# Kernel optimization log

Hardware: AMD Instinct MI355X
Metric: run time of the kernel (lower is better)

Reference implementation:

```python
import jax, jax.numpy as jnp
import numpy as np

INPUT_SIZE = 64
HIDDEN = 128
BATCH = 512
SEQ = 512


def setup_inputs() -> dict:
    key = jax.random.key(0)
    ks = jax.random.split(key, 7)
    s_ih = 1.0 / np.sqrt(HIDDEN)
    token = jax.random.normal(ks[0], (BATCH, SEQ, INPUT_SIZE), dtype=jnp.float32)
    W_ih = jax.random.uniform(ks[1], (HIDDEN, INPUT_SIZE), jnp.float32, -s_ih, s_ih)
    W_hh = jax.random.uniform(ks[2], (HIDDEN, HIDDEN), jnp.float32, -s_ih, s_ih)
    b_ih = jax.random.uniform(ks[3], (HIDDEN,), jnp.float32, -s_ih, s_ih)
    b_hh = jax.random.uniform(ks[4], (HIDDEN,), jnp.float32, -s_ih, s_ih)
    W_lin = jax.random.uniform(ks[5], (1, HIDDEN), jnp.float32, -s_ih, s_ih)
    b_lin = jax.random.uniform(ks[6], (1,), jnp.float32, -s_ih, s_ih)
    return {"token": token, "W_ih": W_ih, "W_hh": W_hh, "b_ih": b_ih,
            "b_hh": b_hh, "W_lin": W_lin, "b_lin": b_lin}


def reference(token, W_ih, W_hh, b_ih, b_hh, W_lin, b_lin):
    # Precompute input projection for all timesteps: [T, B, H]
    x_proj = jnp.einsum('bti,hi->tbh', token, W_ih) + b_ih + b_hh
    h0 = jnp.zeros((token.shape[0], W_hh.shape[0]), dtype=token.dtype)

    def step(h, xp):
        h_new = jnp.tanh(xp + h @ W_hh.T)
        return h_new, None

    h_last, _ = jax.lax.scan(step, h0, x_proj)
    # Linear head on last hidden state: [B, 1]
    return h_last @ W_lin.T + b_lin
```

## Files before the change

kernel.cpp:

```cpp
#include <hip/hip_runtime.h>

#define B_ 512
#define T_ 512
#define I_ 64
#define H_ 128
#define CHUNK 64
#define NCHUNK (T_ / CHUNK)

#define TOKBYTES 16384
#define HB0      (2 * TOKBYTES)
#define HB1      (HB0 + 512)
#define DUMMY    (HB1 + 512)
#define LDS_SZ   (DUMMY + 256)

__device__ __forceinline__ void gload_lds16(const float* g, void* l) {
    __builtin_amdgcn_global_load_lds(
        (const __attribute__((address_space(1))) unsigned int*)g,
        (__attribute__((address_space(3))) unsigned int*)l, 16, 0, 0);
}

#define FM(a, x, w) "v_fmac_f32 v" #a ", v" #x ", v" #w "\n\t"
#define SC(n) "v_mul_f32 v" #n ", 0x4038aa3b, v" #n "\n\t"

#define CLOBS \
    "v48","v49","v50","v51","v52","v53","v54","v55","v56","v57","v58","v59", \
    "v60","v61","v62","v63","v64","v65","v66","v67","v68","v69","v70","v71", \
    "v72","v73","v74","v75","v76","v77","v78","v79","v80","v81","v82","v83", \
    "v84","v85","v86","v87","v88","v89","v90","v91","v92","v93","v94","v95", \
    "v96","v97","v98","v99","v100","v101","v102","v103","v104","v105","v106", \
    "v107","v108","v109","v110","v111","v112","v113","v114","v115","v116", \
    "v117","v118","v119","v120","v121","v122","v123","v124","v125","v126", \
    "v127","memory"

#define RNN_STEP(TOKA, HRD, HWR, BA, BB, BC, BD, M1, M2)                      \
    asm volatile(                                                             \
        "ds_read_b128 v[56:59], %0\n\t"                                       \
        "ds_read_b128 v[64:67], %1\n\t"                                       \
        "ds_read_b128 v[68:71], %1 offset:256\n\t"                            \
        "v_add_u32 %0, 256, %0\n\t"                                           \
        "s_waitcnt lgkmcnt(2)\n\t"                                            \
        "v_fma_f32 v48, v56, v112, %3\n\t"                                    \
        "v_fma_f32 v49, v56, v116, %4\n\t"                                    \
        "v_fma_f32 v50, v56, v120, %5\n\t"                                    \
        "v_fma_f32 v51, v56, v124, %6\n\t"                                    \
        FM(48,57,113) FM(49,57,117) FM(50,57,121) FM(51,57,125)               \
        FM(48,58,114) FM(49,58,118) FM(50,58,122) FM(51,58,126)               \
        FM(48,59,115) FM(49,59,119) FM(50,59,123) FM(51,59,127)               \
        "s_waitcnt lgkmcnt(1)\n\t"                                            \
        FM(48,64,80) FM(49,64,88) FM(50,64,96)  FM(51,64,104)                 \
        FM(48,65,81) FM(49,65,89) FM(50,65,97)  FM(51,65,105)                 \
        FM(48,66,82) FM(49,66,90) FM(50,66,98)  FM(51,66,106)                 \
        FM(48,67,83) FM(49,67,91) FM(50,67,99)  FM(51,67,107)                 \
        "s_waitcnt lgkmcnt(0)\n\t"                                            \
        FM(48,68,84) FM(49,68,92) FM(50,68,100) FM(51,68,108)                 \
        FM(48,69,85) FM(49,69,93) FM(50,69,101) FM(51,69,109)                 \
        FM(48,70,86) FM(49,70,94) FM(50,70,102) FM(51,70,110)                 \
        FM(48,71,87) FM(49,71,95) FM(50,71,103) FM(51,71,111)                 \
        "s_nop 1\n\t"                                                         \
        "v_add_f32 v48, v48, v48 quad_perm:[1,0,3,2] row_mask:0xf bank_mask:0xf\n\t" \
        "v_add_f32 v49, v49, v49 quad_perm:[1,0,3,2] row_mask:0xf bank_mask:0xf\n\t" \
        "v_add_f32 v50, v50, v50 quad_perm:[1,0,3,2] row_mask:0xf bank_mask:0xf\n\t" \
        "v_add_f32 v51, v51, v51 quad_perm:[1,0,3,2] row_mask:0xf bank_mask:0xf\n\t" \
        "v_cndmask_b32 v52, v48, v49, %7\n\t"                                 \
        "v_cndmask_b32 v53, v50, v51, %7\n\t"                                 \
        "s_nop 0\n\t"                                                         \
        "v_add_f32 v52, v52, v52 quad_perm:[2,3,0,1] row_mask:0xf bank_mask:0xf\n\t" \
        "v_add_f32 v53, v53, v53 quad_perm:[2,3,0,1] row_mask:0xf bank_mask:0xf\n\t" \
        "v_cndmask_b32 v54, v52, v53, %8\n\t"                                 \
        "s_nop 1\n\t"                                                         \
        "v_add_f32 v54, v54, v54 row_shl:8 row_mask:0xf bank_mask:0x3\n\t"    \
        "s_nop 1\n\t"                                                         \
        "v_add_f32 v54, v54, v54 row_shl:4 row_mask:0xf bank_mask:0x1\n\t"    \
        "s_nop 1\n\t"                                                         \
        "v_exp_f32 v54, v54\n\t"                                              \
        "s_nop 0\n\t"                                                         \
        "v_add_f32 v54, 1.0, v54\n\t"                                         \
        "v_rcp_f32 v55, v54\n\t"                                              \
        "s_nop 0\n\t"                                                         \
        "v_fma_f32 v54, v55, -2.0, 1.0\n\t"                                   \
        "ds_write_b32 %2, v54\n\t"                                            \
        "s_waitcnt lgkmcnt(0)\n\t"                                            \
        "s_barrier"                                                           \
        : "+v"(TOKA)                                                          \
        : "v"(HRD), "v"(HWR), "v"(BA), "v"(BB), "v"(BC), "v"(BD),             \
          "s"(M1), "s"(M2)                                                    \
        : CLOBS)

__global__ __launch_bounds__(512) __attribute__((amdgpu_waves_per_eu(4, 4)))
void rnn_kernel(const float* __restrict__ token,
                const float* __restrict__ W_ih,
                const float* __restrict__ W_hh,
                const float* __restrict__ b_ih,
                const float* __restrict__ b_hh,
                const float* __restrict__ W_lin,
                const float* __restrict__ b_lin,
                float* __restrict__ out)
{
    __shared__ __align__(16) char lds[LDS_SZ];
    const unsigned lb =
        (unsigned)(uintptr_t)(__attribute__((address_space(3))) char*)lds;

    const int tid = threadIdx.x;
    const int e   = tid & 15;
    const int G   = tid >> 4;
    const int b   = blockIdx.x;
    const int jb  = 4 * G;

    {
        const float* pWh = W_hh + jb * H_ + e * 8;
        const float* pWi = W_ih + jb * I_ + e * 4;
        asm volatile(
            "global_load_dwordx4 v[80:83],   %0, off\n\t"
            "global_load_dwordx4 v[84:87],   %0, off offset:16\n\t"
            "global_load_dwordx4 v[88:91],   %0, off offset:512\n\t"
            "global_load_dwordx4 v[92:95],   %0, off offset:528\n\t"
            "global_load_dwordx4 v[96:99],   %0, off offset:1024\n\t"
            "global_load_dwordx4 v[100:103], %0, off offset:1040\n\t"
            "global_load_dwordx4 v[104:107], %0, off offset:1536\n\t"
            "global_load_dwordx4 v[108:111], %0, off offset:1552\n\t"
            "global_load_dwordx4 v[112:115], %1, off\n\t"
            "global_load_dwordx4 v[116:119], %1, off offset:256\n\t"
            "global_load_dwordx4 v[120:123], %1, off offset:512\n\t"
            "global_load_dwordx4 v[124:127], %1, off offset:768\n\t"
            "s_waitcnt vmcnt(0)\n\t"
            SC(80) SC(81) SC(82) SC(83) SC(84) SC(85) SC(86) SC(87)
            SC(88) SC(89) SC(90) SC(91) SC(92) SC(93) SC(94) SC(95)
            SC(96) SC(97) SC(98) SC(99) SC(100) SC(101) SC(102) SC(103)
            SC(104) SC(105) SC(106) SC(107) SC(108) SC(109) SC(110) SC(111)
            SC(112) SC(113) SC(114) SC(115) SC(116) SC(117) SC(118) SC(119)
            SC(120) SC(121) SC(122) SC(123) SC(124) SC(125) SC(126) SC(127)
            :: "v"(pWh), "v"(pWi) : CLOBS);
    }

    const float k16 = 2.885390081777927f / 16.0f;
    const float biasA = (b_ih[jb + 0] + b_hh[jb + 0]) * k16;
    const float biasB = (b_ih[jb + 1] + b_hh[jb + 1]) * k16;
    const float biasC = (b_ih[jb + 2] + b_hh[jb + 2]) * k16;
    const float biasD = (b_ih[jb + 3] + b_hh[jb + 3]) * k16;
    const unsigned long long M1 = 0xAAAAAAAAAAAAAAAAULL;
    const unsigned long long M2 = 0xCCCCCCCCCCCCCCCCULL;

    const int  jsel   = jb + (e & 3);
    const int  wbyte  = ((((jsel >> 2) & 1) * 16 + (jsel >> 3)) * 16) + (jsel & 3) * 4;
    const bool writer = (e < 4);
    const unsigned dmy = lb + DUMMY + (tid & 63) * 4;
    const unsigned hw0 = writer ? (lb + HB1 + wbyte) : dmy;
    const unsigned hw1 = writer ? (lb + HB0 + wbyte) : dmy;
    const unsigned hr0 = lb + HB0 + e * 16;
    const unsigned hr1 = lb + HB1 + e * 16;

    const float* tok_row = token + (size_t)b * T_ * I_;
    const int S0 = tid, S1 = 512 + tid;

    gload_lds16(tok_row + S0 * 4, lds + S0 * 16);
    gload_lds16(tok_row + S1 * 4, lds + S1 * 16);
    if (tid < H_) *(float*)(lds + HB0 + tid * 4) = 0.0f;
    asm volatile("s_waitcnt vmcnt(0) lgkmcnt(0)\n\ts_barrier" ::: "memory");

#pragma unroll 1
    for (int c = 0; c < NCHUNK; ++c) {
        const int cb = c & 1;
        const bool has_next = (c + 1 < NCHUNK);
        if (has_next) {
            const float* g = tok_row + (size_t)(c + 1) * CHUNK * I_;
            char* dst = lds + (cb ^ 1) * TOKBYTES;
            gload_lds16(g + S0 * 4, dst + S0 * 16);
            gload_lds16(g + S1 * 4, dst + S1 * 16);
        }
        unsigned toka = lb + cb * TOKBYTES + e * 16;

#pragma unroll 1
        for (int tt = 0; tt < CHUNK; tt += 2) {
            RNN_STEP(toka, hr0, hw0, biasA, biasB, biasC, biasD, M1, M2);
            RNN_STEP(toka, hr1, hw1, biasA, biasB, biasC, biasD, M1, M2);
        }

        if (has_next) {
            asm volatile("s_waitcnt vmcnt(0)\n\ts_barrier" ::: "memory");
        }
    }

    if (tid < 64) {
        const int a0 = tid, a1 = tid + 64;
        const int l0 = (((a0 >> 2) & 1) * 16 + (a0 >> 3)) * 4 + (a0 & 3);
        const int l1 = (((a1 >> 2) & 1) * 16 + (a1 >> 3)) * 4 + (a1 & 3);
        float p = *(const float*)(lds + HB0 + l0 * 4) * W_lin[a0]
                + *(const float*)(lds + HB0 + l1 * 4) * W_lin[a1];
#pragma unroll
        for (int off = 32; off; off >>= 1) p += __shfl_down(p, off);
        if (tid == 0) out[b] = p + b_lin[0];
    }
}

extern "C" void kernel_launch(void* const* d_in, const int* in_sizes, int n_in,
                              void* d_out, int out_size, void* d_ws, size_t ws_size,
                              hipStream_t stream) {
    const float* token = (const float*)d_in[0];
    const float* W_ih  = (const float*)d_in[1];
    const float* W_hh  = (const float*)d_in[2];
    const float* b_ih  = (const float*)d_in[3];
    const float* b_hh  = (const float*)d_in[4];
    const float* W_lin = (const float*)d_in[5];
    const float* b_lin = (const float*)d_in[6];
    float* out = (float*)d_out;

    hipLaunchKernelGGL(rnn_kernel, dim3(B_), dim3(512), 0, stream,
                       token, W_ih, W_hh, b_ih, b_hh, W_lin, b_lin, out);
}
```

Before: 206.8 us.

## Stream token inputs directly into registers with a 4-deep global-load ring

Drops the chunked double-buffered global-to-LDS token staging. Each lane now keeps a four-timestep ring of token vectors in VGPRs and issues global_load_dwordx4 directly, waiting on vmcnt(3) so loads run three steps ahead. This removes the per-step LDS token read, the per-chunk barriers and 32KB of LDS. In exchange it exposes per-step global latency, which is only hidden if three steps of prefetch are enough. The offset wraps with a mask, so the last three loads fetch harmless wrapped addresses.

Result: faster. 197.9 us, median of 2 (-4.3%).

```diff
diff --git a/kernel.cpp b/kernel.cpp
--- a/kernel.cpp
+++ b/kernel.cpp
@@ -4,20 +4,11 @@
 #define T_ 512
 #define I_ 64
 #define H_ 128
-#define CHUNK 64
-#define NCHUNK (T_ / CHUNK)
 
-#define TOKBYTES 16384
-#define HB0      (2 * TOKBYTES)
-#define HB1      (HB0 + 512)
-#define DUMMY    (HB1 + 512)
-#define LDS_SZ   (DUMMY + 256)
-
-__device__ __forceinline__ void gload_lds16(const float* g, void* l) {
-    __builtin_amdgcn_global_load_lds(
-        (const __attribute__((address_space(1))) unsigned int*)g,
-        (__attribute__((address_space(3))) unsigned int*)l, 16, 0, 0);
-}
+#define HB0    0
+#define HB1    512
+#define DUMMY  1024
+#define LDS_SZ 1280
 
 #define FM(a, x, w) "v_fmac_f32 v" #a ", v" #x ", v" #w "\n\t"
 #define SC(n) "v_mul_f32 v" #n ", 0x4038aa3b, v" #n "\n\t"
@@ -32,30 +23,31 @@
     "v117","v118","v119","v120","v121","v122","v123","v124","v125","v126", \
     "v127","memory"
 
-#define RNN_STEP(TOKA, HRD, HWR, BA, BB, BC, BD, M1, M2)                      \
+#define RNN_STEP(TA, TB, TC, TD, HRD, HWR)                                    \
     asm volatile(                                                             \
-        "ds_read_b128 v[56:59], %0\n\t"                                       \
-        "ds_read_b128 v[64:67], %1\n\t"                                       \
-        "ds_read_b128 v[68:71], %1 offset:256\n\t"                            \
-        "v_add_u32 %0, 256, %0\n\t"                                           \
-        "s_waitcnt lgkmcnt(2)\n\t"                                            \
-        "v_fma_f32 v48, v56, v112, %3\n\t"                                    \
-        "v_fma_f32 v49, v56, v116, %4\n\t"                                    \
-        "v_fma_f32 v50, v56, v120, %5\n\t"                                    \
-        "v_fma_f32 v51, v56, v124, %6\n\t"                                    \
-        FM(48,57,113) FM(49,57,117) FM(50,57,121) FM(51,57,125)               \
-        FM(48,58,114) FM(49,58,118) FM(50,58,122) FM(51,58,126)               \
-        FM(48,59,115) FM(49,59,119) FM(50,59,123) FM(51,59,127)               \
+        "ds_read_b128 v[72:75], %1\n\t"                                       \
+        "ds_read_b128 v[76:79], %1 offset:256\n\t"                            \
+        "s_waitcnt vmcnt(3)\n\t"                                              \
+        "v_fma_f32 v48, v" #TA ", v112, %3\n\t"                               \
+        "v_fma_f32 v49, v" #TA ", v116, %4\n\t"                               \
+        "v_fma_f32 v50, v" #TA ", v120, %5\n\t"                               \
+        "v_fma_f32 v51, v" #TA ", v124, %6\n\t"                               \
+        FM(48,TB,113) FM(49,TB,117) FM(50,TB,121) FM(51,TB,125)               \
+        FM(48,TC,114) FM(49,TC,118) FM(50,TC,122) FM(51,TC,126)               \
+        FM(48,TD,115) FM(49,TD,119) FM(50,TD,123) FM(51,TD,127)               \
+        "global_load_dwordx4 v[" #TA ":" #TD "], %0, %9\n\t"                  \
+        "v_add_u32 %0, 0x100, %0\n\t"                                         \
+        "v_and_b32 %0, 0x1ffff, %0\n\t"                                       \
         "s_waitcnt lgkmcnt(1)\n\t"                                            \
-        FM(48,64,80) FM(49,64,88) FM(50,64,96)  FM(51,64,104)                 \
-        FM(48,65,81) FM(49,65,89) FM(50,65,97)  FM(51,65,105)                 \
-        FM(48,66,82) FM(49,66,90) FM(50,66,98)  FM(51,66,106)                 \
-        FM(48,67,83) FM(49,67,91) FM(50,67,99)  FM(51,67,107)                 \
+        FM(48,72,80) FM(49,72,88) FM(50,72,96)  FM(51,72,104)                 \
+        FM(48,73,81) FM(49,73,89) FM(50,73,97)  FM(51,73,105)                 \
+        FM(48,74,82) FM(49,74,90) FM(50,74,98)  FM(51,74,106)                 \
+        FM(48,75,83) FM(49,75,91) FM(50,75,99)  FM(51,75,107)                 \
         "s_waitcnt lgkmcnt(0)\n\t"                                            \
-        FM(48,68,84) FM(49,68,92) FM(50,68,100) FM(51,68,108)                 \
-        FM(48,69,85) FM(49,69,93) FM(50,69,101) FM(51,69,109)                 \
-        FM(48,70,86) FM(49,70,94) FM(50,70,102) FM(51,70,110)                 \
-        FM(48,71,87) FM(49,71,95) FM(50,71,103) FM(51,71,111)                 \
+        FM(48,76,84) FM(49,76,92) FM(50,76,100) FM(51,76,108)                 \
+        FM(48,77,85) FM(49,77,93) FM(50,77,101) FM(51,77,109)                 \
+        FM(48,78,86) FM(49,78,94) FM(50,78,102) FM(51,78,110)                 \
+        FM(48,79,87) FM(49,79,95) FM(50,79,103) FM(51,79,111)                 \
         "s_nop 1\n\t"                                                         \
         "v_add_f32 v48, v48, v48 quad_perm:[1,0,3,2] row_mask:0xf bank_mask:0xf\n\t" \
         "v_add_f32 v49, v49, v49 quad_perm:[1,0,3,2] row_mask:0xf bank_mask:0xf\n\t" \
@@ -81,9 +73,9 @@
         "ds_write_b32 %2, v54\n\t"                                            \
         "s_waitcnt lgkmcnt(0)\n\t"                                            \
         "s_barrier"                                                           \
-        : "+v"(TOKA)                                                          \
-        : "v"(HRD), "v"(HWR), "v"(BA), "v"(BB), "v"(BC), "v"(BD),             \
-          "s"(M1), "s"(M2)                                                    \
+        : "+v"(voff)                                                          \
+        : "v"(HRD), "v"(HWR), "v"(biasA), "v"(biasB), "v"(biasC),             \
+          "v"(biasD), "s"(M1), "s"(M2), "s"(sbase)                            \
         : CLOBS)
 
 __global__ __launch_bounds__(512) __attribute__((amdgpu_waves_per_eu(4, 4)))
@@ -150,35 +142,30 @@
     const unsigned hr1 = lb + HB1 + e * 16;
 
     const float* tok_row = token + (size_t)b * T_ * I_;
-    const int S0 = tid, S1 = 512 + tid;
+    const unsigned long long sbase = (unsigned long long)(uintptr_t)tok_row;
 
-    gload_lds16(tok_row + S0 * 4, lds + S0 * 16);
-    gload_lds16(tok_row + S1 * 4, lds + S1 * 16);
+    {
+        const unsigned v0 = e * 16;
+        asm volatile(
+            "global_load_dwordx4 v[56:59], %0, %1\n\t"
+            "global_load_dwordx4 v[60:63], %0, %1 offset:256\n\t"
+            "global_load_dwordx4 v[64:67], %0, %1 offset:512\n\t"
+            "global_load_dwordx4 v[68:71], %0, %1 offset:768\n\t"
+            :: "v"(v0), "s"(sbase) : CLOBS);
+    }
+    unsigned voff = e * 16 + 1024;
     if (tid < H_) *(float*)(lds + HB0 + tid * 4) = 0.0f;
-    asm volatile("s_waitcnt vmcnt(0) lgkmcnt(0)\n\ts_barrier" ::: "memory");
+    asm volatile("s_waitcnt lgkmcnt(0)\n\ts_barrier" ::: "memory");
 
 #pragma unroll 1
-    for (int c = 0; c < NCHUNK; ++c) {
-        const int cb = c & 1;
-        const bool has_next = (c + 1 < NCHUNK);
-        if (has_next) {
-            const float* g = tok_row + (size_t)(c + 1) * CHUNK * I_;
-            char* dst = lds + (cb ^ 1) * TOKBYTES;
-            gload_lds16(g + S0 * 4, dst + S0 * 16);
-            gload_lds16(g + S1 * 4, dst + S1 * 16);
-        }
-        unsigned toka = lb + cb * TOKBYTES + e * 16;
+    for (int t = 0; t < T_; t += 4) {
+        RNN_STEP(56, 57, 58, 59, hr0, hw0);
+        RNN_STEP(60, 61, 62, 63, hr1, hw1);
+        RNN_STEP(64, 65, 66, 67, hr0, hw0);
+        RNN_STEP(68, 69, 70, 71, hr1, hw1);
+    }
 
-#pragma unroll 1
-        for (int tt = 0; tt < CHUNK; tt += 2) {
-            RNN_STEP(toka, hr0, hw0, biasA, biasB, biasC, biasD, M1, M2);
-            RNN_STEP(toka, hr1, hw1, biasA, biasB, biasC, biasD, M1, M2);
-        }
-
-        if (has_next) {
-            asm volatile("s_waitcnt vmcnt(0)\n\ts_barrier" ::: "memory");
-        }
-    }
+    asm volatile("s_waitcnt vmcnt(0)" ::: "memory");
 
     if (tid < 64) {
         const int a0 = tid, a1 = tid + 64;
```
